# Kernel optimization log

Hardware: AMD Instinct MI355X
Metric: run time of the kernel (lower is better)

## Reference

```python
import jax, jax.numpy as jnp
import numpy as np

EPS = 1e-5

def rms_norm(x, scale, eps=EPS):
    rms = jax.lax.rsqrt(jnp.mean(x * x, axis=-1, keepdims=True) + eps)
    return scale * (x * rms)

def act_quant(x, min_scale=0.001, max_scale=1000.0):
    # int8 activation quantization (STE in torch; fwd math only here)
    max_val = jnp.max(jnp.abs(x), axis=-1, keepdims=True)
    s = jnp.clip(127.0 / (max_val + 1e-5), min_scale, max_scale)
    return jnp.clip(jnp.round(s * x), -128.0, 127.0) / s

def weight_quant(w, num_bits=8):
    qmax = 2.0 ** (num_bits - 1) - 1.0
    scale = qmax / (jnp.max(jnp.abs(w)) + 1e-5)
    return jnp.round(jnp.clip(w * scale, -(qmax + 1.0), qmax)) / scale

def ternarize(w):
    sf = jnp.clip(1.0 / (jnp.mean(jnp.abs(w)) + 1e-5), 1e-4, 1e4)
    return jnp.sign(w * sf)

def setup_inputs() -> dict:
    key = jax.random.key(0)
    ks = jax.random.split(key, 5)
    B, S, E, H = 8, 512, 2048, 2048
    x = jax.random.normal(ks[0], (B, S, E), dtype=jnp.float32)
    # ternary {-1,0,1} init as in ternary_initialize
    def tern_init(k, shape):
        r = jax.random.uniform(k, shape, dtype=jnp.float32)
        return jnp.where(r < 1.0 / 3.0, -1.0, jnp.where(r > 2.0 / 3.0, 1.0, 0.0))
    return {
        "x": x,
        "rms_scale": jnp.ones((H,), jnp.float32),
        "W_f": tern_init(ks[1], (E, H)),
        "W_c": tern_init(ks[2], (E, H)),
        "W_g": tern_init(ks[3], (H, E)),
        "b_f": jnp.ones((H,), jnp.float32),
        "b_c": jnp.zeros((H,), jnp.float32),
        "b_g": jnp.zeros((H,), jnp.float32),
    }

def reference(x, rms_scale, W_f, W_c, W_g, b_f, b_c, b_g):
    B, S, E = x.shape
    H = W_f.shape[1]
    # quantize + ternarize weights once (identical every timestep)
    Wt_f = ternarize(weight_quant(W_f))
    Wt_c = ternarize(weight_quant(W_c))
    Wt_g = ternarize(weight_quant(W_g))  # (H, E) but E == H

    def step(h, x_t):
        xq = act_quant(rms_norm(x_t, rms_scale))
        # matmul-free linear: x @ (pos_mask - neg_mask) == x @ sign(W)
        f_t = jax.nn.sigmoid(xq @ Wt_f + b_f)
        c_t = jax.nn.silu(xq @ Wt_c + b_c)
        g_t = jax.nn.sigmoid(xq @ Wt_g + b_g)
        h_new = f_t * h + (1.0 - f_t) * c_t
        o_t = g_t * h_new
        # layer-level copy gate: sigmoid(W_g @ x_t^T)^T = sigmoid(x_t @ W_g^T), raw weights
        cg = jax.nn.sigmoid(x_t @ W_g.T)
        h_out = cg * x_t + (1.0 - cg) * h_new
        return h_out, o_t

    h0 = jnp.zeros((B, H), x.dtype)
    _, outs = jax.lax.scan(step, h0, jnp.swapaxes(x, 0, 1))  # scan over S
    return jnp.swapaxes(outs, 0, 1)  # (B, S, H)
```

## Files before the change

kernel.cpp:

```cpp
#include <hip/hip_runtime.h>
#include <hip/hip_bf16.h>
#include <cstdint>
#include <cstddef>

#define RTOT 4096
#define DIM  2048
#define NCAT 6144
#define NCHUNK 16
#define TCHUNK 32
#define NT 32

typedef __attribute__((ext_vector_type(4))) int int4v;

__device__ __forceinline__ float fast_sigmoid(float z) {
    return __builtin_amdgcn_rcpf(1.0f + __expf(-z));
}
__device__ __forceinline__ unsigned short f2h(float f) {
    union { _Float16 h; unsigned short u; } v; v.h = (_Float16)f; return v.u;
}
__device__ __forceinline__ float h2f(unsigned short u) {
    union { _Float16 h; unsigned short u; } v; v.u = u; return (float)v.h;
}

#define GLDS(gp, lp) __builtin_amdgcn_global_load_lds( \
    (__attribute__((address_space(1))) const void*)(gp), \
    (__attribute__((address_space(3))) void*)(lp), 16, 0, 0)

__device__ __forceinline__ int4v frag_ld(const signed char* p, int R, int lq) {
    return *(const int4v*)(p + R * 64 + ((lq ^ ((R >> 1) & 3)) * 16));
}

__global__ __launch_bounds__(256) void prep_all(
    const float* __restrict__ x, const float* __restrict__ scale,
    const float* __restrict__ Wf, const float* __restrict__ Wc,
    const float* __restrict__ Wg,
    signed char* __restrict__ WcatT, signed char* __restrict__ Wgb,
    signed char* __restrict__ Xq, signed char* __restrict__ Q1,
    signed char* __restrict__ Q2, float* __restrict__ s_arr,
    float* __restrict__ s1_arr)
{
    __shared__ __align__(16) char smem[4224];
    int bid = blockIdx.x;
    int tid = threadIdx.x;
    if (bid < 3072) {
        signed char (*tile)[65] = (signed char(*)[65])smem;
        int j0 = (bid % 96) * 64;
        int k0 = (bid / 96) * 64;
        const float* W = (j0 < 2048) ? Wf : (j0 < 4096) ? Wc : Wg;
        int jb = j0 & 2047;
        int c  = tid & 63;
        int rr = tid >> 6;
#pragma unroll
        for (int p = 0; p < 16; ++p) {
            int kl = p * 4 + rr;
            tile[kl][c] = (signed char)(int)W[(size_t)(k0 + kl) * DIM + jb + c];
        }
        __syncthreads();
#pragma unroll
        for (int p = 0; p < 16; ++p) {
            int jl = p * 4 + rr;
            WcatT[(size_t)(j0 + jl) * DIM + k0 + c] = tile[c][jl];
        }
    } else if (bid < 4096) {
        int idx = (bid - 3072) * 4096 + tid * 16;
#pragma unroll
        for (int p = 0; p < 4; ++p) {
            float4 v = *(const float4*)(Wg + idx + p * 4);
            char4 o;
            o.x = (signed char)(int)v.x; o.y = (signed char)(int)v.y;
            o.z = (signed char)(int)v.z; o.w = (signed char)(int)v.w;
            *(char4*)(Wgb + idx + p * 4) = o;
        }
    } else {
        float* red = (float*)smem;
        float* tot = (float*)(smem + 64);
        int row = bid - 4096;
        const float* xr = x + (size_t)row * DIM + tid * 8;
        const float* sr = scale + tid * 8;
        float4 a0 = *(const float4*)(xr);
        float4 a1 = *(const float4*)(xr + 4);
        float4 c0 = *(const float4*)(sr);
        float4 c1 = *(const float4*)(sr + 4);
        float xs[8] = {a0.x, a0.y, a0.z, a0.w, a1.x, a1.y, a1.z, a1.w};
        float sc[8] = {c0.x, c0.y, c0.z, c0.w, c1.x, c1.y, c1.z, c1.w};
        float sum = 0.f, mx2 = 0.f;
#pragma unroll
        for (int i = 0; i < 8; ++i) {
            sum += xs[i] * xs[i];
            mx2 = fmaxf(mx2, fabsf(xs[i]));
        }
#pragma unroll
        for (int off = 32; off > 0; off >>= 1) {
            sum += __shfl_down(sum, off);
            mx2 = fmaxf(mx2, __shfl_down(mx2, off));
        }
        int lane = tid & 63, wvv = tid >> 6;
        if (lane == 0) { red[wvv] = sum; red[4 + wvv] = mx2; }
        __syncthreads();
        if (tid == 0) {
            tot[0] = red[0] + red[1] + red[2] + red[3];
            tot[1] = fmaxf(fmaxf(red[4], red[5]), fmaxf(red[6], red[7]));
        }
        __syncthreads();
        float rms = 1.0f / sqrtf(tot[0] * (1.0f / 2048.0f) + 1e-5f);
        float y[8]; float mx = 0.f;
#pragma unroll
        for (int i = 0; i < 8; ++i) {
            y[i] = (xs[i] * rms) * sc[i];
            mx = fmaxf(mx, fabsf(y[i]));
        }
#pragma unroll
        for (int off = 32; off > 0; off >>= 1) mx = fmaxf(mx, __shfl_down(mx, off));
        if (lane == 0) red[8 + wvv] = mx;
        __syncthreads();
        if (tid == 0)
            tot[2] = fmaxf(fmaxf(red[8], red[9]), fmaxf(red[10], red[11]));
        __syncthreads();
        float s = 127.0f / (tot[2] + 1e-5f);
        s = fminf(fmaxf(s, 0.001f), 1000.0f);
        float s1 = 127.0f / (tot[1] + 1e-5f);
        float inv_s1 = 1.0f / s1;
        if (tid == 0) { s_arr[row] = s; s1_arr[row] = s1; }
        signed char q8[8], q1b[8], q2b[8];
#pragma unroll
        for (int i = 0; i < 8; ++i) {
            float q = fminf(fmaxf(rintf(s * y[i]), -128.f), 127.f);
            q8[i] = (signed char)(int)q;
            float qq1 = fminf(fmaxf(rintf(s1 * xs[i]), -128.f), 127.f);
            q1b[i] = (signed char)(int)qq1;
            float r = xs[i] - qq1 * inv_s1;
            float qq2 = fminf(fmaxf(rintf(s1 * 256.f * r), -128.f), 127.f);
            q2b[i] = (signed char)(int)qq2;
        }
        size_t o = (size_t)row * DIM + tid * 8;
        *(int2*)(Xq + o) = *(int2*)q8;
        *(int2*)(Q1 + o) = *(int2*)q1b;
        *(int2*)(Q2 + o) = *(int2*)q2b;
    }
}

__global__ __launch_bounds__(512, 2) void gemm_all(
    const signed char* __restrict__ Xq, const signed char* __restrict__ WcatT,
    const signed char* __restrict__ Q1, const signed char* __restrict__ Q2,
    const signed char* __restrict__ Wgb,
    const float* __restrict__ s_arr, const float* __restrict__ s1_arr,
    const float* __restrict__ b_f, const float* __restrict__ b_c,
    const float* __restrict__ b_g,
    unsigned short* __restrict__ FCG,
    unsigned short* __restrict__ U,
    unsigned short* __restrict__ V)
{
    extern __shared__ __align__(16) signed char lds[];
    int bid = blockIdx.x;
    int grp = bid / 5, r5 = bid % 5;
    int tid = threadIdx.x;
    int lane = tid & 63, wv = tid >> 6;
    int lr = lane & 15, lq = lane >> 4;
    int srow = wv * 16 + (lane >> 2);
    int ssw  = ((lane & 3) ^ ((srow >> 1) & 3)) * 16;
    const size_t ustep = (size_t)128 * DIM;

    if (r5 < 3) {
        int fb = grp * 3 + r5;
        int m0 = (fb & 15) * 256;
        int n0 = (fb >> 4) * 256;
        int wm = (wv >> 2) * 128;
        int wn = (wv & 3) * 64;
        const signed char* Ab = Xq + (size_t)m0 * DIM;
        const signed char* Bb = WcatT + (size_t)n0 * DIM;
        const signed char* gA = Ab + (size_t)srow * DIM + ssw;
        const signed char* gB = Bb + (size_t)srow * DIM + ssw;

        int4v acc[8][4] = {};
        int4v a[4], b[4];

#pragma unroll
        for (int t0 = 0; t0 < 2; ++t0) {
            signed char* sb = lds + t0 * 32768;
            GLDS(gA + t0 * 64,         sb + wv * 1024);
            GLDS(gA + ustep + t0 * 64, sb + 8192 + wv * 1024);
            GLDS(gB + t0 * 64,         sb + 16384 + wv * 1024);
            GLDS(gB + ustep + t0 * 64, sb + 16384 + 8192 + wv * 1024);
        }

        int bc = 0, bn = 1, bs = 2;
        for (int t = 0; t < NT; ++t) {
            if (t == NT - 1) { asm volatile("s_waitcnt vmcnt(0)" ::: "memory"); }
            else             { asm volatile("s_waitcnt vmcnt(4)" ::: "memory"); }
            __builtin_amdgcn_sched_barrier(0);
            __builtin_amdgcn_s_barrier();
            __builtin_amdgcn_sched_barrier(0);
            const signed char* cA = lds + bc * 32768;
            const signed char* cB = cA + 16384;
            signed char* sA = lds + bs * 32768;
            signed char* sB = sA + 16384;
            int kt2 = (t + 2) * 64;
            bool st = (t + 2 < NT);

#pragma unroll
            for (int i = 0; i < 4; ++i) a[i] = frag_ld(cA, wm + i * 16 + lr, lq);
#pragma unroll
            for (int j = 0; j < 4; ++j) b[j] = frag_ld(cB, wn + j * 16 + lr, lq);
            if (st) {
                GLDS(gA + kt2,         sA + wv * 1024);
                GLDS(gA + ustep + kt2, sA + 8192 + wv * 1024);
            }
            __builtin_amdgcn_s_barrier();
            asm volatile("s_waitcnt lgkmcnt(0)" ::: "memory");
            __builtin_amdgcn_sched_barrier(0);
            __builtin_amdgcn_s_setprio(1);
#pragma unroll
            for (int i = 0; i < 4; ++i)
#pragma unroll
                for (int j = 0; j < 4; ++j)
                    acc[i][j] = __builtin_amdgcn_mfma_i32_16x16x64_i8(
                        a[i], b[j], acc[i][j], 0, 0, 0);
            __builtin_amdgcn_s_setprio(0);
            __builtin_amdgcn_s_barrier();

#pragma unroll
            for (int i = 0; i < 4; ++i) a[i] = frag_ld(cA, wm + (4 + i) * 16 + lr, lq);
            if (st) {
                GLDS(gB + kt2,         sB + wv * 1024);
                GLDS(gB + ustep + kt2, sB + 8192 + wv * 1024);
            }
            __builtin_amdgcn_s_barrier();
            asm volatile("s_waitcnt lgkmcnt(0)" ::: "memory");
            __builtin_amdgcn_sched_barrier(0);
            __builtin_amdgcn_s_setprio(1);
#pragma unroll
            for (int i = 0; i < 4; ++i)
#pragma unroll
                for (int j = 0; j < 4; ++j)
                    acc[4 + i][j] = __builtin_amdgcn_mfma_i32_16x16x64_i8(
                        a[i], b[j], acc[4 + i][j], 0, 0, 0);
            __builtin_amdgcn_s_setprio(0);
            __builtin_amdgcn_s_barrier();

            int tmp = bc; bc = bn; bn = bs; bs = tmp;
        }

        int rowb = m0 + wm;
#pragma unroll
        for (int mi = 0; mi < 8; ++mi) {
            float rinv[4];
#pragma unroll
            for (int r = 0; r < 4; ++r)
                rinv[r] = __builtin_amdgcn_rcpf(s_arr[rowb + mi * 16 + lq * 4 + r]);
#pragma unroll
            for (int ni = 0; ni < 4; ++ni) {
                int gcol = n0 + wn + ni * 16 + lr;
                int sec = gcol >> 11;
                int jj = gcol & 2047;
                float bias = (sec == 0) ? b_f[jj] : (sec == 1) ? b_c[jj] : b_g[jj];
#pragma unroll
                for (int r = 0; r < 4; ++r) {
                    int grow = rowb + mi * 16 + lq * 4 + r;
                    float z = fmaf((float)acc[mi][ni][r], rinv[r], bias);
                    float sg = fast_sigmoid(z);
                    FCG[(size_t)grow * NCAT + gcol] = f2h((sec == 1) ? z * sg : sg);
                }
            }
        }
    } else {
        int cb = grp * 2 + (r5 - 3);
        int m0 = (cb & 15) * 256;
        int n0 = (cb >> 4) * 128;
        int wm = (wv >> 2) * 128;
        int wn = (wv & 3) * 32;
        const signed char* A1b = Q1 + (size_t)m0 * DIM;
        const signed char* A2b = Q2 + (size_t)m0 * DIM;
        const signed char* Bb  = Wgb + (size_t)n0 * DIM;
        const signed char* g1 = A1b + (size_t)srow * DIM + ssw;
        const signed char* g2 = A2b + (size_t)srow * DIM + ssw;
        const signed char* gB = Bb + (size_t)srow * DIM + ssw;

        int4v acc1[8][2] = {};
        int4v acc2[8][2] = {};
        int4v a1[8], a2[8], b[2];

#pragma unroll
        for (int t0 = 0; t0 < 2; ++t0) {
            signed char* sb = lds + t0 * 40960;
            GLDS(g1 + t0 * 64,         sb + wv * 1024);
            GLDS(g1 + ustep + t0 * 64, sb + 8192 + wv * 1024);
            GLDS(gB + t0 * 64,         sb + 32768 + wv * 1024);
            GLDS(g2 + t0 * 64,         sb + 16384 + wv * 1024);
            GLDS(g2 + ustep + t0 * 64, sb + 16384 + 8192 + wv * 1024);
        }

        int bc = 0, bn = 1, bs = 2;
        for (int t = 0; t < NT; ++t) {
            if (t == NT - 1) { asm volatile("s_waitcnt vmcnt(0)" ::: "memory"); }
            else             { asm volatile("s_waitcnt vmcnt(5)" ::: "memory"); }
            __builtin_amdgcn_sched_barrier(0);
            __builtin_amdgcn_s_barrier();
            __builtin_amdgcn_sched_barrier(0);
            const signed char* cA1 = lds + bc * 40960;
            const signed char* cA2 = cA1 + 16384;
            const signed char* cB  = cA1 + 32768;
            signed char* s1p = lds + bs * 40960;
            signed char* s2p = s1p + 16384;
            signed char* sBp = s1p + 32768;
            int kt2 = (t + 2) * 64;
            bool st = (t + 2 < NT);

#pragma unroll
            for (int i = 0; i < 8; ++i) a1[i] = frag_ld(cA1, wm + i * 16 + lr, lq);
#pragma unroll
            for (int j = 0; j < 2; ++j) b[j] = frag_ld(cB, wn + j * 16 + lr, lq);
            if (st) {
                GLDS(g1 + kt2,         s1p + wv * 1024);
                GLDS(g1 + ustep + kt2, s1p + 8192 + wv * 1024);
                GLDS(gB + kt2,         sBp + wv * 1024);
            }
            __builtin_amdgcn_s_barrier();
            asm volatile("s_waitcnt lgkmcnt(0)" ::: "memory");
            __builtin_amdgcn_sched_barrier(0);
            __builtin_amdgcn_s_setprio(1);
#pragma unroll
            for (int i = 0; i < 8; ++i)
#pragma unroll
                for (int j = 0; j < 2; ++j)
                    acc1[i][j] = __builtin_amdgcn_mfma_i32_16x16x64_i8(
                        a1[i], b[j], acc1[i][j], 0, 0, 0);
            __builtin_amdgcn_s_setprio(0);
            __builtin_amdgcn_s_barrier();

#pragma unroll
            for (int i = 0; i < 8; ++i) a2[i] = frag_ld(cA2, wm + i * 16 + lr, lq);
            if (st) {
                GLDS(g2 + kt2,         s2p + wv * 1024);
                GLDS(g2 + ustep + kt2, s2p + 8192 + wv * 1024);
            }
            __builtin_amdgcn_s_barrier();
            asm volatile("s_waitcnt lgkmcnt(0)" ::: "memory");
            __builtin_amdgcn_sched_barrier(0);
            __builtin_amdgcn_s_setprio(1);
#pragma unroll
            for (int i = 0; i < 8; ++i)
#pragma unroll
                for (int j = 0; j < 2; ++j)
                    acc2[i][j] = __builtin_amdgcn_mfma_i32_16x16x64_i8(
                        a2[i], b[j], acc2[i][j], 0, 0, 0);
            __builtin_amdgcn_s_setprio(0);
            __builtin_amdgcn_s_barrier();

            int tmp = bc; bc = bn; bn = bs; bs = tmp;
        }

        int rowb = m0 + wm;
#pragma unroll
        for (int mi = 0; mi < 8; ++mi) {
            float rinv[4];
#pragma unroll
            for (int r = 0; r < 4; ++r)
                rinv[r] = __builtin_amdgcn_rcpf(s1_arr[rowb + mi * 16 + lq * 4 + r]);
#pragma unroll
            for (int ni = 0; ni < 2; ++ni) {
                int gcol = n0 + wn + ni * 16 + lr;
#pragma unroll
                for (int r = 0; r < 4; ++r) {
                    int grow = rowb + mi * 16 + lq * 4 + r;
                    size_t go = (size_t)grow * DIM + gcol;
                    float zs = (float)acc1[mi][ni][r] + (float)acc2[mi][ni][r] * (1.f / 256.f);
                    float cg = fast_sigmoid(zs * rinv[r]);
                    float xv = ((float)Q1[go] + (float)Q2[go] * (1.f / 256.f)) * rinv[r];
                    U[go] = f2h(cg * xv);
                    V[go] = f2h(1.f - cg);
                }
            }
        }
    }
}

__global__ __launch_bounds__(256) void scan_partial(
    const unsigned short* __restrict__ FCG, const unsigned short* __restrict__ U,
    const unsigned short* __restrict__ V, float4* __restrict__ PQ4)
{
    int tp = blockIdx.x * 256 + threadIdx.x;
    int c = blockIdx.y;
    int b = blockIdx.z;
    int h0 = tp * 2;
    size_t r0 = (size_t)(b * 512 + c * TCHUNK);
    const unsigned short* fp = FCG + r0 * NCAT + h0;
    const unsigned short* up = U + r0 * DIM + h0;
    const unsigned short* vp = V + r0 * DIM + h0;
    float P0 = 1.f, Q0 = 0.f, P1 = 1.f, Q1v = 0.f;
#pragma unroll 4
    for (int t = 0; t < TCHUNK; ++t) {
        unsigned fw = *(const unsigned*)(fp);
        unsigned cw = *(const unsigned*)(fp + 2048);
        unsigned uw = *(const unsigned*)(up);
        unsigned vw = *(const unsigned*)(vp);
        float f0 = h2f(fw & 0xffff), f1 = h2f(fw >> 16);
        float c0 = h2f(cw & 0xffff), c1 = h2f(cw >> 16);
        float u0 = h2f(uw & 0xffff), u1 = h2f(uw >> 16);
        float v0 = h2f(vw & 0xffff), v1 = h2f(vw >> 16);
        float A0 = v0 * f0, A1 = v1 * f1;
        float B0 = fmaf(v0 * (1.f - f0), c0, u0);
        float B1 = fmaf(v1 * (1.f - f1), c1, u1);
        P0 = A0 * P0; Q0 = fmaf(A0, Q0, B0);
        P1 = A1 * P1; Q1v = fmaf(A1, Q1v, B1);
        fp += NCAT; up += DIM; vp += DIM;
    }
    float4 o; o.x = P0; o.y = Q0; o.z = P1; o.w = Q1v;
    PQ4[(size_t)c * 8192 + b * 1024 + tp] = o;
}

__global__ __launch_bounds__(256) void scan_final(
    const unsigned short* __restrict__ FCG, const unsigned short* __restrict__ U,
    const unsigned short* __restrict__ V, const float4* __restrict__ PQ4,
    float* __restrict__ out)
{
    int tp = blockIdx.x * 256 + threadIdx.x;
    int c = blockIdx.y;
    int b = blockIdx.z;
    int h0 = tp * 2;
    float h0s = 0.f, h1s = 0.f;
    for (int cc = 0; cc < c; ++cc) {
        float4 pq = PQ4[(size_t)cc * 8192 + b * 1024 + tp];
        h0s = fmaf(pq.x, h0s, pq.y);
        h1s = fmaf(pq.z, h1s, pq.w);
    }
    size_t r0 = (size_t)(b * 512 + c * TCHUNK);
    const unsigned short* fp = FCG + r0 * NCAT + h0;
    const unsigned short* up = U + r0 * DIM + h0;
    const unsigned short* vp = V + r0 * DIM + h0;
    float* op = out + r0 * DIM + h0;
#pragma unroll 4
    for (int t = 0; t < TCHUNK; ++t) {
        unsigned fw = *(const unsigned*)(fp);
        unsigned cw = *(const unsigned*)(fp + 2048);
        unsigned gw = *(const unsigned*)(fp + 4096);
        unsigned uw = *(const unsigned*)(up);
        unsigned vw = *(const unsigned*)(vp);
        float f0 = h2f(fw & 0xffff), f1 = h2f(fw >> 16);
        float c0 = h2f(cw & 0xffff), c1 = h2f(cw >> 16);
        float g0 = h2f(gw & 0xffff), g1 = h2f(gw >> 16);
        float u0 = h2f(uw & 0xffff), u1 = h2f(uw >> 16);
        float v0 = h2f(vw & 0xffff), v1 = h2f(vw >> 16);
        float hn0 = f0 * h0s + (1.f - f0) * c0;
        float hn1 = f1 * h1s + (1.f - f1) * c1;
        float2 ov; ov.x = g0 * hn0; ov.y = g1 * hn1;
        *(float2*)op = ov;
        h0s = fmaf(v0, hn0, u0);
        h1s = fmaf(v1, hn1, u1);
        fp += NCAT; up += DIM; vp += DIM; op += DIM;
    }
}

extern "C" void kernel_launch(void* const* d_in, const int* in_sizes, int n_in,
                              void* d_out, int out_size, void* d_ws, size_t ws_size,
                              hipStream_t stream) {
    const float* x     = (const float*)d_in[0];
    const float* rmssc = (const float*)d_in[1];
    const float* W_f   = (const float*)d_in[2];
    const float* W_c   = (const float*)d_in[3];
    const float* W_g   = (const float*)d_in[4];
    const float* b_f   = (const float*)d_in[5];
    const float* b_c   = (const float*)d_in[6];
    const float* b_g   = (const float*)d_in[7];
    float* out = (float*)d_out;

    char* ws = (char*)d_ws;
    size_t off = 0;
    auto alloc = [&](size_t bytes) -> void* {
        void* p = ws + off;
        off += (bytes + 255) & ~(size_t)255;
        return p;
    };
    signed char* WcatT = (signed char*)alloc((size_t)NCAT * DIM);
    signed char* Wgb   = (signed char*)alloc((size_t)DIM * DIM);
    signed char* Xq    = (signed char*)alloc((size_t)RTOT * DIM);
    signed char* Q1    = (signed char*)alloc((size_t)RTOT * DIM);
    signed char* Q2    = (signed char*)alloc((size_t)RTOT * DIM);
    float* s_arr       = (float*)alloc((size_t)RTOT * 4);
    float* s1_arr      = (float*)alloc((size_t)RTOT * 4);
    unsigned short* FCG = (unsigned short*)alloc((size_t)RTOT * NCAT * 2);
    unsigned short* U   = (unsigned short*)alloc((size_t)RTOT * DIM * 2);
    unsigned short* V   = (unsigned short*)alloc((size_t)RTOT * DIM * 2);
    float4* PQ4        = (float4*)alloc((size_t)NCHUNK * 8192 * 16);

    static int gemm_attr_once = [](){
        return (int)hipFuncSetAttribute((const void*)gemm_all,
                   hipFuncAttributeMaxDynamicSharedMemorySize, 3 * 40960);
    }();
    (void)gemm_attr_once;

    hipLaunchKernelGGL(prep_all, dim3(8192), dim3(256), 0, stream,
                       x, rmssc, W_f, W_c, W_g, WcatT, Wgb, Xq, Q1, Q2,
                       s_arr, s1_arr);
    hipLaunchKernelGGL(gemm_all, dim3(640), dim3(512), 3 * 40960, stream,
                       Xq, WcatT, Q1, Q2, Wgb, s_arr, s1_arr,
                       b_f, b_c, b_g, FCG, U, V);
    hipLaunchKernelGGL(scan_partial, dim3(DIM / 512, NCHUNK, 8), dim3(256), 0, stream,
                       FCG, U, V, PQ4);
    hipLaunchKernelGGL(scan_final, dim3(DIM / 512, NCHUNK, 8), dim3(256), 0, stream,
                       FCG, U, V, PQ4, out);
}
```

Measured before the change: 275.4 us.

## Use one wavefront per row in prep, finer scan chunks, skip last partial

The activation-quant part of prep_all now gives each 64-lane wavefront a whole row. Reductions become xor shuffles inside the wave, which removes the LDS round-trips and __syncthreads, and the grid drops from 8192 to 5120 blocks. The chunked scan switches to 32 chunks of 16 timesteps for more parallelism, and scan_partial no longer launches the final chunk, whose carry is never consumed. This trades a longer serial carry loop in scan_final (partly unrolled) and higher register use per thread in prep.

```diff
diff --git a/kernel.cpp b/kernel.cpp
--- a/kernel.cpp
+++ b/kernel.cpp
@@ -6,8 +6,8 @@
 #define RTOT 4096
 #define DIM  2048
 #define NCAT 6144
-#define NCHUNK 16
-#define TCHUNK 32
+#define NCHUNK 32
+#define TCHUNK 16
 #define NT 32
 
 typedef __attribute__((ext_vector_type(4))) int int4v;
@@ -72,70 +72,72 @@
             *(char4*)(Wgb + idx + p * 4) = o;
         }
     } else {
-        float* red = (float*)smem;
-        float* tot = (float*)(smem + 64);
-        int row = bid - 4096;
-        const float* xr = x + (size_t)row * DIM + tid * 8;
-        const float* sr = scale + tid * 8;
-        float4 a0 = *(const float4*)(xr);
-        float4 a1 = *(const float4*)(xr + 4);
-        float4 c0 = *(const float4*)(sr);
-        float4 c1 = *(const float4*)(sr + 4);
-        float xs[8] = {a0.x, a0.y, a0.z, a0.w, a1.x, a1.y, a1.z, a1.w};
-        float sc[8] = {c0.x, c0.y, c0.z, c0.w, c1.x, c1.y, c1.z, c1.w};
+        int row = (bid - 4096) * 4 + (tid >> 6);
+        int lane = tid & 63;
+        const float* xr = x + (size_t)row * DIM;
+        float xs[32], ys[32];
         float sum = 0.f, mx2 = 0.f;
 #pragma unroll
-        for (int i = 0; i < 8; ++i) {
+        for (int sw = 0; sw < 4; ++sw) {
+            int base = sw * 512 + lane * 8;
+            float4 a0 = *(const float4*)(xr + base);
+            float4 a1 = *(const float4*)(xr + base + 4);
+            xs[sw * 8 + 0] = a0.x; xs[sw * 8 + 1] = a0.y;
+            xs[sw * 8 + 2] = a0.z; xs[sw * 8 + 3] = a0.w;
+            xs[sw * 8 + 4] = a1.x; xs[sw * 8 + 5] = a1.y;
+            xs[sw * 8 + 6] = a1.z; xs[sw * 8 + 7] = a1.w;
+        }
+#pragma unroll
+        for (int i = 0; i < 32; ++i) {
             sum += xs[i] * xs[i];
             mx2 = fmaxf(mx2, fabsf(xs[i]));
         }
 #pragma unroll
-        for (int off = 32; off > 0; off >>= 1) {
-            sum += __shfl_down(sum, off);
-            mx2 = fmaxf(mx2, __shfl_down(mx2, off));
-        }
-        int lane = tid & 63, wvv = tid >> 6;
-        if (lane == 0) { red[wvv] = sum; red[4 + wvv] = mx2; }
-        __syncthreads();
-        if (tid == 0) {
-            tot[0] = red[0] + red[1] + red[2] + red[3];
-            tot[1] = fmaxf(fmaxf(red[4], red[5]), fmaxf(red[6], red[7]));
-        }
-        __syncthreads();
-        float rms = 1.0f / sqrtf(tot[0] * (1.0f / 2048.0f) + 1e-5f);
-        float y[8]; float mx = 0.f;
-#pragma unroll
-        for (int i = 0; i < 8; ++i) {
-            y[i] = (xs[i] * rms) * sc[i];
-            mx = fmaxf(mx, fabsf(y[i]));
-        }
-#pragma unroll
-        for (int off = 32; off > 0; off >>= 1) mx = fmaxf(mx, __shfl_down(mx, off));
-        if (lane == 0) red[8 + wvv] = mx;
-        __syncthreads();
-        if (tid == 0)
-            tot[2] = fmaxf(fmaxf(red[8], red[9]), fmaxf(red[10], red[11]));
-        __syncthreads();
-        float s = 127.0f / (tot[2] + 1e-5f);
+        for (int off = 1; off < 64; off <<= 1) {
+            sum += __shfl_xor(sum, off);
+            mx2 = fmaxf(mx2, __shfl_xor(mx2, off));
+        }
+        float rms = 1.0f / sqrtf(sum * (1.0f / 2048.0f) + 1e-5f);
+        float mx = 0.f;
+#pragma unroll
+        for (int sw = 0; sw < 4; ++sw) {
+            int base = sw * 512 + lane * 8;
+            float4 c0 = *(const float4*)(scale + base);
+            float4 c1 = *(const float4*)(scale + base + 4);
+            float scv[8] = {c0.x, c0.y, c0.z, c0.w, c1.x, c1.y, c1.z, c1.w};
+#pragma unroll
+            for (int i = 0; i < 8; ++i) {
+                float yv = (xs[sw * 8 + i] * rms) * scv[i];
+                ys[sw * 8 + i] = yv;
+                mx = fmaxf(mx, fabsf(yv));
+            }
+        }
+#pragma unroll
+        for (int off = 1; off < 64; off <<= 1) mx = fmaxf(mx, __shfl_xor(mx, off));
+        float s = 127.0f / (mx + 1e-5f);
         s = fminf(fmaxf(s, 0.001f), 1000.0f);
-        float s1 = 127.0f / (tot[1] + 1e-5f);
+        float s1 = 127.0f / (mx2 + 1e-5f);
         float inv_s1 = 1.0f / s1;
-        if (tid == 0) { s_arr[row] = s; s1_arr[row] = s1; }
-        signed char q8[8], q1b[8], q2b[8];
-#pragma unroll
-        for (int i = 0; i < 8; ++i) {
-            float q = fminf(fmaxf(rintf(s * y[i]), -128.f), 127.f);
-            q8[i] = (signed char)(int)q;
-            float qq1 = fminf(fmaxf(rintf(s1 * xs[i]), -128.f), 127.f);
-            q1b[i] = (signed char)(int)qq1;
-            float r = xs[i] - qq1 * inv_s1;
-            float qq2 = fminf(fmaxf(rintf(s1 * 256.f * r), -128.f), 127.f);
-            q2b[i] = (signed char)(int)qq2;
-        }
-        size_t o = (size_t)row * DIM + tid * 8;
-        *(int2*)(Xq + o) = *(int2*)q8;
-        *(int2*)(Q1 + o) = *(int2*)q1b;
-        *(int2*)(Q2 + o) = *(int2*)q2b;
+        if (lane == 0) { s_arr[row] = s; s1_arr[row] = s1; }
+#pragma unroll
+        for (int sw = 0; sw < 4; ++sw) {
+            signed char q8[8], q1b[8], q2b[8];
+#pragma unroll
+            for (int i = 0; i < 8; ++i) {
+                float xv = xs[sw * 8 + i];
+                float q = fminf(fmaxf(rintf(s * ys[sw * 8 + i]), -128.f), 127.f);
+                q8[i] = (signed char)(int)q;
+                float qq1 = fminf(fmaxf(rintf(s1 * xv), -128.f), 127.f);
+                q1b[i] = (signed char)(int)qq1;
+                float r = xv - qq1 * inv_s1;
+                float qq2 = fminf(fmaxf(rintf(s1 * 256.f * r), -128.f), 127.f);
+                q2b[i] = (signed char)(int)qq2;
+            }
+            size_t o = (size_t)row * DIM + sw * 512 + lane * 8;
+            *(int2*)(Xq + o) = *(int2*)q8;
+            *(int2*)(Q1 + o) = *(int2*)q1b;
+            *(int2*)(Q2 + o) = *(int2*)q2b;
+        }
     }
 }
 
@@ -418,6 +420,7 @@
     int b = blockIdx.z;
     int h0 = tp * 2;
     float h0s = 0.f, h1s = 0.f;
+#pragma unroll 4
     for (int cc = 0; cc < c; ++cc) {
         float4 pq = PQ4[(size_t)cc * 8192 + b * 1024 + tp];
         h0s = fmaf(pq.x, h0s, pq.y);
@@ -488,13 +491,13 @@
     }();
     (void)gemm_attr_once;
 
-    hipLaunchKernelGGL(prep_all, dim3(8192), dim3(256), 0, stream,
+    hipLaunchKernelGGL(prep_all, dim3(5120), dim3(256), 0, stream,
                        x, rmssc, W_f, W_c, W_g, WcatT, Wgb, Xq, Q1, Q2,
                        s_arr, s1_arr);
     hipLaunchKernelGGL(gemm_all, dim3(640), dim3(512), 3 * 40960, stream,
                        Xq, WcatT, Q1, Q2, Wgb, s_arr, s1_arr,
                        b_f, b_c, b_g, FCG, U, V);
-    hipLaunchKernelGGL(scan_partial, dim3(DIM / 512, NCHUNK, 8), dim3(256), 0, stream,
+    hipLaunchKernelGGL(scan_partial, dim3(DIM / 512, NCHUNK - 1, 8), dim3(256), 0, stream,
                        FCG, U, V, PQ4);
     hipLaunchKernelGGL(scan_final, dim3(DIM / 512, NCHUNK, 8), dim3(256), 0, stream,
                        FCG, U, V, PQ4, out);
```

Measured after the change: 275.3 us. Within noise of the previous version (-0.0%).
